# Kernel tuning notes

Hardware: AMD Instinct MI355X
Metric: run time of the kernel (lower is better)

The kernel has to match this reference:

```python
import jax, jax.numpy as jnp
import numpy as np

N, F, H, K = 4096, 512, 256, 8
NEG = -1e9


def _attention(h, mask, a_w, a_b):
    # h: [N,H]; mask: [N,N] bool; a_w: [K,2H]; a_b: [K]
    # per-head logits[i,j] = lrelu(a_src . h_i + a_dst . h_j + b), softmax over
    # neighbors j (A[i,j]==1); out_i = h_i + sum_j alpha_ij h_j; isolated nodes
    # (no neighbors) keep h_i unchanged (alpha row masked to zero).
    Hd = h.shape[1]
    src = h @ a_w[:, :Hd].T + a_b[None, :]   # [N,K]
    dst = h @ a_w[:, Hd:].T                  # [N,K]
    fmask = mask.astype(h.dtype)
    outs = []
    for k in range(a_w.shape[0]):
        logits = jax.nn.leaky_relu(src[:, k][:, None] + dst[:, k][None, :], 0.01)
        logits = jnp.where(mask, logits, NEG)
        alpha = jax.nn.softmax(logits, axis=1) * fmask  # zero rows for isolated nodes
        outs.append(h + alpha @ h)
    return outs


def setup_inputs() -> dict:
    key = jax.random.key(0)
    ks = jax.random.split(key, 12)
    s = 0.02
    adjacency = jax.random.randint(ks[0], (N, N), 0, 2).astype(jnp.float32)
    feats = jax.random.normal(ks[1], (N, F), dtype=jnp.float32)
    return {
        "adjacency": adjacency,
        "feats": feats,
        "W1_w": jax.random.normal(ks[2], (H, F), dtype=jnp.float32) * s,
        "W1_b": jnp.zeros((H,), jnp.float32),
        "a1_w": jax.random.normal(ks[3], (K, 2 * H), dtype=jnp.float32) * s,
        "a1_b": jnp.zeros((K,), jnp.float32),
        "W2_w": jax.random.normal(ks[4], (H, K * H), dtype=jnp.float32) * s,
        "W2_b": jnp.zeros((H,), jnp.float32),
        "a2_w": jax.random.normal(ks[5], (K, 2 * H), dtype=jnp.float32) * s,
        "a2_b": jnp.zeros((K,), jnp.float32),
        "out_w": jax.random.normal(ks[6], (1, H), dtype=jnp.float32) * s,
        "out_b": jnp.zeros((1,), jnp.float32),
    }


def reference(adjacency, feats, W1_w, W1_b, a1_w, a1_b, W2_w, W2_b, a2_w, a2_b, out_w, out_b):
    mask = adjacency == 1.0
    # torch.inner(A, feats.T) == A @ feats; dropout is identity in eval mode
    h1 = (adjacency @ feats) @ W1_w.T + W1_b            # [N,H]
    heads1 = _attention(h1, mask, a1_w, a1_b)           # K x [N,H]
    h1_new = jax.nn.elu(jnp.concatenate(heads1, axis=1))  # [N,K*H]
    h2 = h1_new @ W2_w.T + W2_b                         # [N,H]
    heads2 = _attention(h2, mask, a2_w, a2_b)
    avg = sum(heads2) / a2_w.shape[0]                   # [N,H]
    h2_new = jax.nn.elu(avg)
    avgd = jnp.mean(h2_new, axis=0)                     # [H]
    return avgd @ out_w.T + out_b                       # [1]
```

## Files before the change

kernel.cpp:

```cpp
#include <hip/hip_runtime.h>
#include <hip/hip_bf16.h>
#include <hip/hip_fp16.h>


#define NN 4096
#define FF 512
#define HH 256
#define KK 8
#define KH 2048

typedef __attribute__((ext_vector_type(8))) short bf16x8;
typedef __attribute__((ext_vector_type(4))) float f32x4;
typedef __attribute__((ext_vector_type(16))) float f32x16;
typedef _Float16 h16x2 __attribute__((ext_vector_type(2)));
typedef _Float16 h16x8 __attribute__((ext_vector_type(8)));

__device__ inline short f2bf(float x) {
    __hip_bfloat16 b = __float2bfloat16(x);
    return *reinterpret_cast<short*>(&b);
}
__device__ inline short to_bf(float x) { return f2bf(x); }
__device__ inline short to_bf(short x) { return x; }

__device__ inline unsigned int pkh(float a, float b) {
    auto r = __builtin_amdgcn_cvt_pkrtz(a, b);
    unsigned int u;
    __builtin_memcpy(&u, &r, 4);
    return u;
}
__device__ inline unsigned int h2mul(unsigned int a, unsigned int b) {
    h16x2 av, bv;
    __builtin_memcpy(&av, &a, 4);
    __builtin_memcpy(&bv, &b, 4);
    h16x2 r = av * bv;
    unsigned int u;
    __builtin_memcpy(&u, &r, 4);
    return u;
}
__device__ inline unsigned int h2max(unsigned int a, unsigned int b) {
    h16x2 av, bv;
    __builtin_memcpy(&av, &a, 4);
    __builtin_memcpy(&bv, &b, 4);
    h16x2 r = __builtin_elementwise_max(av, bv);
    unsigned int u;
    __builtin_memcpy(&u, &r, 4);
    return u;
}
__device__ inline float h2dot1(unsigned int a, float c) {
    h16x2 av;
    __builtin_memcpy(&av, &a, 4);
    h16x2 one = {(_Float16)1.0f, (_Float16)1.0f};
    return __builtin_amdgcn_fdot2(av, one, c, false);
}

__device__ inline unsigned int enc_f(float x) {
    unsigned int u = __float_as_uint(x);
    return (u & 0x80000000u) ? ~u : (u | 0x80000000u);
}
__device__ inline float dec_f(unsigned int e) {
    unsigned int u = (e & 0x80000000u) ? (e ^ 0x80000000u) : ~e;
    return __uint_as_float(u);
}

__global__ void pack_mask_kernel(const float* __restrict__ adj,
                                 unsigned int* __restrict__ mbits) {
    int i = blockIdx.x;
    int lane = threadIdx.x & 63;
    int wv = threadIdx.x >> 6;
    for (int j0 = wv * 64; j0 < NN; j0 += 256) {
        float v = adj[(size_t)i * NN + j0 + lane];
        unsigned long long b = __ballot(v == 1.0f);
        if (lane == 0) {
            mbits[i * 128 + (j0 >> 5)]     = (unsigned int)(b & 0xffffffffull);
            mbits[i * 128 + (j0 >> 5) + 1] = (unsigned int)(b >> 32);
        }
    }
}

template <typename T>
__global__ __launch_bounds__(256) void cvt_a_frag_kernel(const T* __restrict__ src,
                                                         bf16x8* __restrict__ dst, int K) {
    int t = threadIdx.x, lane = t & 63, w = t >> 6, mt = blockIdx.x;
    int Kt = K >> 5;
    int m = mt * 16 + (lane & 15), kq = (lane >> 4) * 8;
    for (int kt = w; kt < Kt; kt += 4) {
        size_t base = (size_t)m * K + kt * 32 + kq;
        bf16x8 v;
#pragma unroll
        for (int jj = 0; jj < 8; jj++) v[jj] = to_bf(src[base + jj]);
        dst[((size_t)mt * Kt + kt) * 64 + lane] = v;
    }
}

__global__ __launch_bounds__(256) void cvt_bt_frag_kernel(const float* __restrict__ Wm,
                                                          bf16x8* __restrict__ dst,
                                                          int K, int Nt) {
    int t = threadIdx.x, lane = t & 63, w = t >> 6, nt = blockIdx.x;
    int Kt = K >> 5;
    int n = nt * 16 + (lane & 15), kq = (lane >> 4) * 8;
    for (int kt = w; kt < Kt; kt += 4) {
        size_t base = (size_t)n * K + kt * 32 + kq;
        bf16x8 v;
#pragma unroll
        for (int jj = 0; jj < 8; jj++) v[jj] = f2bf(Wm[base + jj]);
        dst[((size_t)kt * Nt + nt) * 64 + lane] = v;
    }
}

template <int W>
__global__ __launch_bounds__(256) void cvt_b_frag_kernel(const float* __restrict__ src,
                                                         bf16x8* __restrict__ dst) {
    __shared__ float hs[32][W + 8];
    constexpr int Nt = W / 16;
    int t = threadIdx.x, jb = blockIdx.x;
    {
        int r = t >> 3, cb = (t & 7) * (W / 8);
        const float* sp = &src[(size_t)(jb * 32 + r) * W + cb];
#pragma unroll
        for (int q = 0; q < W / 32; q++) *(float4*)&hs[r][cb + q * 4] = *(const float4*)&sp[q * 4];
    }
    __syncthreads();
    for (int id = t; id < Nt * 64; id += 256) {
        int nt = id >> 6, lane = id & 63;
        int c = nt * 16 + (lane & 15), q8 = (lane >> 4) * 8;
        bf16x8 v;
#pragma unroll
        for (int jj = 0; jj < 8; jj++) v[jj] = f2bf(hs[q8 + jj][c]);
        dst[((size_t)jb * Nt + nt) * 64 + lane] = v;
    }
}

__global__ __launch_bounds__(256) void gemm_frag_kernel(
    const bf16x8* __restrict__ Af, const bf16x8* __restrict__ Bf,
    const float* __restrict__ bias, float* __restrict__ C,
    int Kt, int Nt, int Nrow) {
    int t = threadIdx.x, lane = t & 63, w = t >> 6;
    int quad = lane >> 4, c16 = lane & 15;
    int wm = w & 1, wn = w >> 1;
    int mt0 = blockIdx.y * 4 + wm * 2;
    int nt0 = blockIdx.x * 8 + wn * 4;
    f32x4 acc[2][4];
#pragma unroll
    for (int i = 0; i < 2; i++)
#pragma unroll
        for (int j = 0; j < 4; j++) acc[i][j] = (f32x4){0.f, 0.f, 0.f, 0.f};
    const bf16x8* ap = Af + (size_t)mt0 * Kt * 64 + lane;
    const bf16x8* bp = Bf + (size_t)nt0 * 64 + lane;
#pragma unroll 2
    for (int kt = 0; kt < Kt; kt++) {
        bf16x8 a0 = ap[(size_t)kt * 64];
        bf16x8 a1 = ap[((size_t)Kt + kt) * 64];
        bf16x8 b0 = bp[(size_t)kt * Nt * 64];
        bf16x8 b1 = bp[((size_t)kt * Nt + 1) * 64];
        bf16x8 b2 = bp[((size_t)kt * Nt + 2) * 64];
        bf16x8 b3 = bp[((size_t)kt * Nt + 3) * 64];
        acc[0][0] = __builtin_amdgcn_mfma_f32_16x16x32_bf16(a0, b0, acc[0][0], 0, 0, 0);
        acc[0][1] = __builtin_amdgcn_mfma_f32_16x16x32_bf16(a0, b1, acc[0][1], 0, 0, 0);
        acc[0][2] = __builtin_amdgcn_mfma_f32_16x16x32_bf16(a0, b2, acc[0][2], 0, 0, 0);
        acc[0][3] = __builtin_amdgcn_mfma_f32_16x16x32_bf16(a0, b3, acc[0][3], 0, 0, 0);
        acc[1][0] = __builtin_amdgcn_mfma_f32_16x16x32_bf16(a1, b0, acc[1][0], 0, 0, 0);
        acc[1][1] = __builtin_amdgcn_mfma_f32_16x16x32_bf16(a1, b1, acc[1][1], 0, 0, 0);
        acc[1][2] = __builtin_amdgcn_mfma_f32_16x16x32_bf16(a1, b2, acc[1][2], 0, 0, 0);
        acc[1][3] = __builtin_amdgcn_mfma_f32_16x16x32_bf16(a1, b3, acc[1][3], 0, 0, 0);
    }
#pragma unroll
    for (int i = 0; i < 2; i++) {
#pragma unroll
        for (int j = 0; j < 4; j++) {
            int n = (nt0 + j) * 16 + c16;
            float bv = bias ? bias[n] : 0.f;
#pragma unroll
            for (int reg = 0; reg < 4; reg++) {
                int m = (mt0 + i) * 16 + quad * 4 + reg;
                C[(size_t)m * Nrow + n] = acc[i][j][reg] + bv;
            }
        }
    }
}

__global__ __launch_bounds__(256) void gemm_adj_kernel(
    const unsigned int* __restrict__ mbits, const bf16x8* __restrict__ Bf,
    float* __restrict__ C, int Kt, int Nt, int Nrow) {
    int t = threadIdx.x, lane = t & 63, w = t >> 6;
    int quad = lane >> 4, c16 = lane & 15;
    int wm = w & 1, wn = w >> 1;
    int mt0 = blockIdx.y * 4 + wm * 2;
    int nt0 = blockIdx.x * 8 + wn * 4;
    int m = lane & 15, q8 = (lane >> 4) * 8;
    int row0 = mt0 * 16 + m, row1 = row0 + 16;
    f32x4 acc[2][4];
#pragma unroll
    for (int i = 0; i < 2; i++)
#pragma unroll
        for (int j = 0; j < 4; j++) acc[i][j] = (f32x4){0.f, 0.f, 0.f, 0.f};
    const bf16x8* bp = Bf + (size_t)nt0 * 64 + lane;
#pragma unroll 2
    for (int kt = 0; kt < Kt; kt++) {
        unsigned int w0 = mbits[(size_t)row0 * 128 + kt];
        unsigned int w1 = mbits[(size_t)row1 * 128 + kt];
        unsigned int mb0 = (w0 >> q8) & 0xffu;
        unsigned int mb1 = (w1 >> q8) & 0xffu;
        union { unsigned int u[4]; bf16x8 v; } A0, A1;
#pragma unroll
        for (int jp = 0; jp < 4; jp++) {
            unsigned int u0 = (mb0 >> (2 * jp)) & 3u;
            unsigned int u1 = (mb1 >> (2 * jp)) & 3u;
            A0.u[jp] = ((u0 * 0x8001u) & 0x10001u) * 0x3F80u;
            A1.u[jp] = ((u1 * 0x8001u) & 0x10001u) * 0x3F80u;
        }
        bf16x8 b0 = bp[(size_t)kt * Nt * 64];
        bf16x8 b1 = bp[((size_t)kt * Nt + 1) * 64];
        bf16x8 b2 = bp[((size_t)kt * Nt + 2) * 64];
        bf16x8 b3 = bp[((size_t)kt * Nt + 3) * 64];
        acc[0][0] = __builtin_amdgcn_mfma_f32_16x16x32_bf16(A0.v, b0, acc[0][0], 0, 0, 0);
        acc[0][1] = __builtin_amdgcn_mfma_f32_16x16x32_bf16(A0.v, b1, acc[0][1], 0, 0, 0);
        acc[0][2] = __builtin_amdgcn_mfma_f32_16x16x32_bf16(A0.v, b2, acc[0][2], 0, 0, 0);
        acc[0][3] = __builtin_amdgcn_mfma_f32_16x16x32_bf16(A0.v, b3, acc[0][3], 0, 0, 0);
        acc[1][0] = __builtin_amdgcn_mfma_f32_16x16x32_bf16(A1.v, b0, acc[1][0], 0, 0, 0);
        acc[1][1] = __builtin_amdgcn_mfma_f32_16x16x32_bf16(A1.v, b1, acc[1][1], 0, 0, 0);
        acc[1][2] = __builtin_amdgcn_mfma_f32_16x16x32_bf16(A1.v, b2, acc[1][2], 0, 0, 0);
        acc[1][3] = __builtin_amdgcn_mfma_f32_16x16x32_bf16(A1.v, b3, acc[1][3], 0, 0, 0);
    }
#pragma unroll
    for (int i = 0; i < 2; i++) {
#pragma unroll
        for (int j = 0; j < 4; j++) {
            int n = (nt0 + j) * 16 + c16;
#pragma unroll
            for (int reg = 0; reg < 4; reg++) {
                int mm = (mt0 + i) * 16 + quad * 4 + reg;
                C[(size_t)mm * Nrow + n] = acc[i][j][reg];
            }
        }
    }
}

__global__ __launch_bounds__(256) void prep_kernel(const float* __restrict__ h,
                                                   const float* __restrict__ aw,
                                                   const float* __restrict__ ab,
                                                   h16x8* __restrict__ HB16,
                                                   float* __restrict__ srcT,
                                                   float* __restrict__ dstT,
                                                   unsigned int* __restrict__ maxd_u) {
    __shared__ __align__(16) float hs[32][264];
    __shared__ __align__(16) float awl[KK * 512];
    int t = threadIdx.x, jb = blockIdx.x;
#pragma unroll
    for (int q = 0; q < 4; q++)
        *(float4*)&awl[(t + q * 256) * 4] = *(const float4*)&aw[(t + q * 256) * 4];
    {
        int r = t >> 3, cb = (t & 7) * 32;
        const float* hp = &h[(size_t)(jb * 32 + r) * HH + cb];
#pragma unroll
        for (int q = 0; q < 8; q++) *(float4*)&hs[r][cb + q * 4] = *(const float4*)&hp[q * 4];
    }
    __syncthreads();
#pragma unroll
    for (int it = 0; it < 4; it++) {
        int id = t + it * 256;
        int q = id >> 9, nt = (id >> 6) & 7, lane = id & 63;
        int c = nt * 32 + (lane & 31), j8 = q * 16 + (lane >> 5) * 8;
        union { unsigned int u[4]; h16x8 v; } pk;
#pragma unroll
        for (int jp = 0; jp < 4; jp++)
            pk.u[jp] = pkh(hs[j8 + 2 * jp][c], hs[j8 + 2 * jp + 1][c]);
        HB16[((size_t)(jb * 2 + q)) * 512 + nt * 64 + lane] = pk.v;
    }
    {
        const float LOG2E = 1.4426950408889634f;
        int row = t & 31, head = t >> 5;
        float s = ab[head], d = 0.f;
        const float* ws = &awl[head * 512];
        const float* wd = ws + 256;
#pragma unroll 4
        for (int c = 0; c < 256; c += 4) {
            float4 hv = *(const float4*)&hs[row][c];
            float4 a4 = *(const float4*)&ws[c];
            float4 b4 = *(const float4*)&wd[c];
            s += hv.x * a4.x + hv.y * a4.y + hv.z * a4.z + hv.w * a4.w;
            d += hv.x * b4.x + hv.y * b4.y + hv.z * b4.z + hv.w * b4.w;
        }
        float ds = d * LOG2E;
        srcT[head * NN + jb * 32 + row] = s * LOG2E;
        dstT[head * NN + jb * 32 + row] = ds;
        float mx = ds;
#pragma unroll
        for (int off = 16; off > 0; off >>= 1) mx = fmaxf(mx, __shfl_xor(mx, off));
        if (row == 0) atomicMax(&maxd_u[head], enc_f(mx));
    }
}

template <int MODE>
__global__ __launch_bounds__(256, 2) void attn32_kernel(
    const float* __restrict__ h, const float* __restrict__ srcT,
    const float* __restrict__ dstT, const unsigned int* __restrict__ maxd_u,
    const unsigned int* __restrict__ mbits, const h16x8* __restrict__ HB16,
    void* __restrict__ outp) {
    __shared__ __align__(16) char smraw[49600];
    __shared__ float l_all[2][2][32];
    __shared__ float linv_l[2][32];
    unsigned short* e1t = (unsigned short*)smraw;
    unsigned short* e2t = (unsigned short*)(smraw + 16384);
    unsigned int* mrow = (unsigned int*)(smraw + 32768);
    float* accbuf = (float*)smraw;

    int t = threadIdx.x;
    int i0 = blockIdx.x * 32;
    int k0 = blockIdx.y * 2;

    float Dv0 = dec_f(maxd_u[k0]), Dv1 = dec_f(maxd_u[k0 + 1]);
#pragma unroll
    for (int q = 0; q < 8; q++) {
        int idx = t + q * 256;
        int hh = idx >> 10, off = (idx & 1023) * 4;
        float D = hh ? Dv1 : Dv0;
        float4 dv = *(const float4*)&dstT[(size_t)(k0 + hh) * NN + off];
        float d0 = dv.x - D, d1 = dv.y - D, d2 = dv.z - D, d3 = dv.w - D;
        uint2 p1, p2;
        p1.x = pkh(__builtin_amdgcn_exp2f(d0), __builtin_amdgcn_exp2f(d1));
        p1.y = pkh(__builtin_amdgcn_exp2f(d2), __builtin_amdgcn_exp2f(d3));
        p2.x = pkh(__builtin_amdgcn_exp2f(0.01f * d0), __builtin_amdgcn_exp2f(0.01f * d1));
        p2.y = pkh(__builtin_amdgcn_exp2f(0.01f * d2), __builtin_amdgcn_exp2f(0.01f * d3));
        *(uint2*)&e1t[hh * 4096 + off] = p1;
        *(uint2*)&e2t[hh * 4096 + off] = p2;
    }
#pragma unroll
    for (int q = 0; q < 16; q++) {
        int idx = t + q * 256;
        int r = idx >> 7, wd = idx & 127;
        mrow[r * 131 + wd] = mbits[(size_t)(i0 + r) * 128 + wd];
    }
    __syncthreads();

    int lane = t & 63, w = t >> 6;
    int jh = w & 1, ch = w >> 1;
    int rowl = lane & 31, jsub = (lane >> 5) * 8;

    unsigned int AcPk[2], BcPk[2];
    float lacc[2] = {0.f, 0.f};
#pragma unroll
    for (int hh = 0; hh < 2; hh++) {
        float sL = srcT[(size_t)(k0 + hh) * NN + i0 + rowl];
        float xm = sL + (hh ? Dv1 : Dv0);
        float mL = fmaxf(xm, 0.01f * xm);
        float Acf = __builtin_amdgcn_exp2f(xm - mL);
        float Bcf = __builtin_amdgcn_exp2f(fmaf(0.01f, xm, -mL));
        AcPk[hh] = pkh(Acf, Acf);
        BcPk[hh] = pkh(Bcf, Bcf);
    }

    f32x16 acc[2][4];
#pragma unroll
    for (int hh = 0; hh < 2; hh++)
#pragma unroll
        for (int nt = 0; nt < 4; nt++)
#pragma unroll
            for (int r = 0; r < 16; r++) acc[hh][nt][r] = 0.f;

    const unsigned short* e1b0 = e1t;
    const unsigned short* e1b1 = e1t + 4096;
    const unsigned short* e2b0 = e2t;
    const unsigned short* e2b1 = e2t + 4096;

    for (int jj0 = 0; jj0 < 64; jj0++) {
        int jbg = jh * 64 + jj0;
        unsigned int word = mrow[rowl * 131 + jbg];
#pragma unroll
        for (int s = 0; s < 2; s++) {
            int j16 = jbg * 2 + s;
            unsigned int mb = (word >> (s * 16 + jsub)) & 0xffu;
            unsigned int mw[4];
#pragma unroll
            for (int jp = 0; jp < 4; jp++) {
                unsigned int u2 = (mb >> (2 * jp)) & 3u;
                mw[jp] = ((u2 * 0x8001u) & 0x10001u) * 0xffffu;
            }
            int eoff = j16 * 16 + jsub;
            union { unsigned int u[4]; h16x8 v; } P[2];
            {
                uint4 E1 = *(const uint4*)&e1b0[eoff];
                uint4 E2 = *(const uint4*)&e2b0[eoff];
                unsigned int v0 = h2max(h2mul(E1.x, AcPk[0]), h2mul(E2.x, BcPk[0])) & mw[0];
                unsigned int v1 = h2max(h2mul(E1.y, AcPk[0]), h2mul(E2.y, BcPk[0])) & mw[1];
                unsigned int v2 = h2max(h2mul(E1.z, AcPk[0]), h2mul(E2.z, BcPk[0])) & mw[2];
                unsigned int v3 = h2max(h2mul(E1.w, AcPk[0]), h2mul(E2.w, BcPk[0])) & mw[3];
                lacc[0] = h2dot1(v0, lacc[0]);
                lacc[0] = h2dot1(v1, lacc[0]);
                lacc[0] = h2dot1(v2, lacc[0]);
                lacc[0] = h2dot1(v3, lacc[0]);
                P[0].u[0] = v0; P[0].u[1] = v1; P[0].u[2] = v2; P[0].u[3] = v3;
            }
            {
                uint4 E1 = *(const uint4*)&e1b1[eoff];
                uint4 E2 = *(const uint4*)&e2b1[eoff];
                unsigned int v0 = h2max(h2mul(E1.x, AcPk[1]), h2mul(E2.x, BcPk[1])) & mw[0];
                unsigned int v1 = h2max(h2mul(E1.y, AcPk[1]), h2mul(E2.y, BcPk[1])) & mw[1];
                unsigned int v2 = h2max(h2mul(E1.z, AcPk[1]), h2mul(E2.z, BcPk[1])) & mw[2];
                unsigned int v3 = h2max(h2mul(E1.w, AcPk[1]), h2mul(E2.w, BcPk[1])) & mw[3];
                lacc[1] = h2dot1(v0, lacc[1]);
                lacc[1] = h2dot1(v1, lacc[1]);
                lacc[1] = h2dot1(v2, lacc[1]);
                lacc[1] = h2dot1(v3, lacc[1]);
                P[1].u[0] = v0; P[1].u[1] = v1; P[1].u[2] = v2; P[1].u[3] = v3;
            }
            const h16x8* bp = &HB16[(size_t)j16 * 512 + (ch * 4) * 64 + lane];
#pragma unroll
            for (int nt = 0; nt < 4; nt++) {
                h16x8 bv = bp[nt * 64];
                acc[0][nt] = __builtin_amdgcn_mfma_f32_32x32x16_f16(P[0].v, bv, acc[0][nt], 0, 0, 0);
                acc[1][nt] = __builtin_amdgcn_mfma_f32_32x32x16_f16(P[1].v, bv, acc[1][nt], 0, 0, 0);
            }
        }
    }

    lacc[0] += __shfl_xor(lacc[0], 32);
    lacc[1] += __shfl_xor(lacc[1], 32);
    if (ch == 0 && lane < 32) {
        l_all[jh][0][lane] = lacc[0];
        l_all[jh][1][lane] = lacc[1];
    }
    __syncthreads();
    if (t < 32) {
#pragma unroll
        for (int hh = 0; hh < 2; hh++) {
            float lt = l_all[0][hh][t] + l_all[1][hh][t];
            linv_l[hh][t] = (lt > 0.f) ? 1.f / lt : 0.f;
        }
    }
    __syncthreads();

#pragma unroll
    for (int r = 0; r < 2; r++) {
        if (jh == 1) {
#pragma unroll
            for (int nt = 0; nt < 4; nt++) {
                float* dp = accbuf + (size_t)((ch * 4 + nt) * 16) * 64 + lane;
#pragma unroll
                for (int reg = 0; reg < 16; reg++) dp[reg * 64] = acc[r][nt][reg];
            }
        }
        __syncthreads();
        if (jh == 0) {
            int khead = k0 + r;
#pragma unroll
            for (int nt = 0; nt < 4; nt++) {
                const float* sp = accbuf + (size_t)((ch * 4 + nt) * 16) * 64 + lane;
                int c = (ch * 4 + nt) * 32 + (lane & 31);
#pragma unroll
                for (int reg = 0; reg < 16; reg++) {
                    int rowloc = (reg & 3) + 8 * (reg >> 2) + 4 * (lane >> 5);
                    float v = (acc[r][nt][reg] + sp[reg * 64]) * linv_l[r][rowloc];
                    int i = i0 + rowloc;
                    if (MODE == 1) {
                        v += h[(size_t)i * HH + c];
                        v = (v > 0.f) ? v : (__expf(v) - 1.f);
                        ((short*)outp)[(size_t)i * KH + (size_t)khead * HH + c] = f2bf(v);
                    } else {
                        ((short*)outp)[(size_t)khead * NN * HH + (size_t)i * HH + c] = f2bf(v);
                    }
                }
            }
        }
        if (r == 0) __syncthreads();
    }
}

__global__ void colsum_kernel(const float* __restrict__ h2,
                              const short* __restrict__ heads,
                              float* __restrict__ partial) {
    int c = threadIdx.x;
    int b = blockIdx.x;
    float s = 0.f;
    for (int il = 0; il < 64; il++) {
        int i = b * 64 + il;
        float v = h2[(size_t)i * HH + c];
#pragma unroll
        for (int k = 0; k < KK; k++) {
            unsigned int bits = (unsigned int)(unsigned short)heads[(size_t)k * NN * HH + (size_t)i * HH + c];
            v += 0.125f * __uint_as_float(bits << 16);
        }
        s += (v > 0.f) ? v : (__expf(v) - 1.f);
    }
    partial[b * HH + c] = s;
}

__global__ void final_kernel(const float* __restrict__ partial,
                             const float* __restrict__ out_w,
                             const float* __restrict__ out_b,
                             float* __restrict__ dout) {
    __shared__ float red[256];
    int c = threadIdx.x;
    float s = 0.f;
    for (int b = 0; b < 64; b++) s += partial[b * HH + c];
    red[c] = (s / 4096.f) * out_w[c];
    __syncthreads();
    for (int off = 128; off > 0; off >>= 1) {
        if (c < off) red[c] += red[c + off];
        __syncthreads();
    }
    if (c == 0) dout[0] = red[0] + out_b[0];
}

extern "C" void kernel_launch(void* const* d_in, const int* in_sizes, int n_in,
                              void* d_out, int out_size, void* d_ws, size_t ws_size,
                              hipStream_t stream) {
    (void)in_sizes; (void)n_in; (void)out_size; (void)ws_size;
    const float* adj   = (const float*)d_in[0];
    const float* feats = (const float*)d_in[1];
    const float* W1_w  = (const float*)d_in[2];
    const float* W1_b  = (const float*)d_in[3];
    const float* a1_w  = (const float*)d_in[4];
    const float* a1_b  = (const float*)d_in[5];
    const float* W2_w  = (const float*)d_in[6];
    const float* W2_b  = (const float*)d_in[7];
    const float* a2_w  = (const float*)d_in[8];
    const float* a2_b  = (const float*)d_in[9];
    const float* out_w = (const float*)d_in[10];
    const float* out_b = (const float*)d_in[11];

    char* w = (char*)d_ws;
    const size_t MB = 1ull << 20;
    unsigned int* mbits = (unsigned int*)(w);
    short*  h1nb   = (short*)(w + 2 * MB);
    bf16x8* h1na   = (bf16x8*)(w + 18 * MB);
    short*  planes = (short*)(w + 2 * MB);
    bf16x8* Bfeats = (bf16x8*)(w + 34 * MB);
    float*  h2     = (float*)(w + 34 * MB);
    float*  tmp1   = (float*)(w + 38 * MB);
    float*  h1     = (float*)(w + 38 * MB);
    bf16x8* W1f    = (bf16x8*)(w + 42 * MB);
    bf16x8* W2f    = (bf16x8*)(w + 42 * MB + 256 * 1024);
    float*  srcT   = (float*)(w + 43 * MB + 256 * 1024);
    float*  dstT   = (float*)(w + 43 * MB + 384 * 1024);
    unsigned int* maxd_u = (unsigned int*)(w + 43 * MB + 512 * 1024);
    h16x8*  HB16   = (h16x8*)(w + 44 * MB);
    bf16x8* tmp1a  = (bf16x8*)(w + 46 * MB);
    float*  partial = (float*)(w + 50 * MB);

    pack_mask_kernel<<<NN, 256, 0, stream>>>(adj, mbits);
    cvt_b_frag_kernel<FF><<<NN / 32, 256, 0, stream>>>(feats, Bfeats);
    gemm_adj_kernel<<<dim3(FF / 128, NN / 64), 256, 0, stream>>>(
        mbits, Bfeats, tmp1, NN / 32, FF / 16, FF);
    cvt_a_frag_kernel<float><<<NN / 16, 256, 0, stream>>>(tmp1, tmp1a, FF);
    cvt_bt_frag_kernel<<<HH / 16, 256, 0, stream>>>(W1_w, W1f, FF, HH / 16);
    gemm_frag_kernel<<<dim3(HH / 128, NN / 64), 256, 0, stream>>>(
        tmp1a, W1f, W1_b, h1, FF / 32, HH / 16, HH);

    (void)hipMemsetAsync(maxd_u, 0, KK * sizeof(unsigned int), stream);
    prep_kernel<<<NN / 32, 256, 0, stream>>>(h1, a1_w, a1_b, HB16, srcT, dstT, maxd_u);
    attn32_kernel<1><<<dim3(NN / 32, KK / 2), 256, 0, stream>>>(
        h1, srcT, dstT, maxd_u, mbits, HB16, h1nb);
    cvt_a_frag_kernel<short><<<NN / 16, 256, 0, stream>>>(h1nb, h1na, KH);
    cvt_bt_frag_kernel<<<HH / 16, 256, 0, stream>>>(W2_w, W2f, KH, HH / 16);
    gemm_frag_kernel<<<dim3(HH / 128, NN / 64), 256, 0, stream>>>(
        h1na, W2f, W2_b, h2, KH / 32, HH / 16, HH);

    (void)hipMemsetAsync(maxd_u, 0, KK * sizeof(unsigned int), stream);
    prep_kernel<<<NN / 32, 256, 0, stream>>>(h2, a2_w, a2_b, HB16, srcT, dstT, maxd_u);
    attn32_kernel<2><<<dim3(NN / 32, KK / 2), 256, 0, stream>>>(
        h2, srcT, dstT, maxd_u, mbits, HB16, planes);
    colsum_kernel<<<64, 256, 0, stream>>>(h2, planes, partial);
    final_kernel<<<1, 256, 0, stream>>>(partial, out_w, out_b, (float*)d_out);
}
```

Baseline: 462.8 us.

## Process one attention head per block instead of two; widen colsum grid

The attention kernel now handles a single head per block and launches twice as many blocks (grid y = K instead of K/2). Each block needs half the LDS for the exp tables and half the accumulator registers, which should allow more occupancy and more parallel blocks. The cost is that the mask row load and the HB16 B-fragment loads are no longer shared across two heads, so global/LDS traffic per MFMA roughly doubles. The colsum reduction also uses 256 blocks of 16 rows instead of 64 blocks of 64 rows, with the final kernel summing 256 partials.

```diff
diff --git a/kernel.cpp b/kernel.cpp
--- a/kernel.cpp
+++ b/kernel.cpp
@@ -296,33 +296,32 @@
     const float* __restrict__ dstT, const unsigned int* __restrict__ maxd_u,
     const unsigned int* __restrict__ mbits, const h16x8* __restrict__ HB16,
     void* __restrict__ outp) {
-    __shared__ __align__(16) char smraw[49600];
-    __shared__ float l_all[2][2][32];
-    __shared__ float linv_l[2][32];
+    __shared__ __align__(16) char smraw[33536];
+    __shared__ float l_all[2][32];
+    __shared__ float linv_l[32];
     unsigned short* e1t = (unsigned short*)smraw;
-    unsigned short* e2t = (unsigned short*)(smraw + 16384);
-    unsigned int* mrow = (unsigned int*)(smraw + 32768);
+    unsigned short* e2t = (unsigned short*)(smraw + 8192);
+    unsigned int* mrow = (unsigned int*)(smraw + 16384);
     float* accbuf = (float*)smraw;
 
     int t = threadIdx.x;
     int i0 = blockIdx.x * 32;
-    int k0 = blockIdx.y * 2;
-
-    float Dv0 = dec_f(maxd_u[k0]), Dv1 = dec_f(maxd_u[k0 + 1]);
-#pragma unroll
-    for (int q = 0; q < 8; q++) {
+    int khead = blockIdx.y;
+
+    float Dv = dec_f(maxd_u[khead]);
+#pragma unroll
+    for (int q = 0; q < 4; q++) {
         int idx = t + q * 256;
-        int hh = idx >> 10, off = (idx & 1023) * 4;
-        float D = hh ? Dv1 : Dv0;
-        float4 dv = *(const float4*)&dstT[(size_t)(k0 + hh) * NN + off];
-        float d0 = dv.x - D, d1 = dv.y - D, d2 = dv.z - D, d3 = dv.w - D;
+        int off = idx * 4;
+        float4 dv = *(const float4*)&dstT[(size_t)khead * NN + off];
+        float d0 = dv.x - Dv, d1 = dv.y - Dv, d2 = dv.z - Dv, d3 = dv.w - Dv;
         uint2 p1, p2;
         p1.x = pkh(__builtin_amdgcn_exp2f(d0), __builtin_amdgcn_exp2f(d1));
         p1.y = pkh(__builtin_amdgcn_exp2f(d2), __builtin_amdgcn_exp2f(d3));
         p2.x = pkh(__builtin_amdgcn_exp2f(0.01f * d0), __builtin_amdgcn_exp2f(0.01f * d1));
         p2.y = pkh(__builtin_amdgcn_exp2f(0.01f * d2), __builtin_amdgcn_exp2f(0.01f * d3));
-        *(uint2*)&e1t[hh * 4096 + off] = p1;
-        *(uint2*)&e2t[hh * 4096 + off] = p2;
+        *(uint2*)&e1t[off] = p1;
+        *(uint2*)&e2t[off] = p2;
     }
 #pragma unroll
     for (int q = 0; q < 16; q++) {
@@ -336,31 +335,23 @@
     int jh = w & 1, ch = w >> 1;
     int rowl = lane & 31, jsub = (lane >> 5) * 8;
 
-    unsigned int AcPk[2], BcPk[2];
-    float lacc[2] = {0.f, 0.f};
-#pragma unroll
-    for (int hh = 0; hh < 2; hh++) {
-        float sL = srcT[(size_t)(k0 + hh) * NN + i0 + rowl];
-        float xm = sL + (hh ? Dv1 : Dv0);
+    unsigned int AcPk, BcPk;
+    float lacc = 0.f;
+    {
+        float sL = srcT[(size_t)khead * NN + i0 + rowl];
+        float xm = sL + Dv;
         float mL = fmaxf(xm, 0.01f * xm);
         float Acf = __builtin_amdgcn_exp2f(xm - mL);
         float Bcf = __builtin_amdgcn_exp2f(fmaf(0.01f, xm, -mL));
-        AcPk[hh] = pkh(Acf, Acf);
-        BcPk[hh] = pkh(Bcf, Bcf);
-    }
-
-    f32x16 acc[2][4];
-#pragma unroll
-    for (int hh = 0; hh < 2; hh++)
-#pragma unroll
-        for (int nt = 0; nt < 4; nt++)
-#pragma unroll
-            for (int r = 0; r < 16; r++) acc[hh][nt][r] = 0.f;
-
-    const unsigned short* e1b0 = e1t;
-    const unsigned short* e1b1 = e1t + 4096;
-    const unsigned short* e2b0 = e2t;
-    const unsigned short* e2b1 = e2t + 4096;
+        AcPk = pkh(Acf, Acf);
+        BcPk = pkh(Bcf, Bcf);
+    }
+
+    f32x16 acc[4];
+#pragma unroll
+    for (int nt = 0; nt < 4; nt++)
+#pragma unroll
+        for (int r = 0; r < 16; r++) acc[nt][r] = 0.f;
 
     for (int jj0 = 0; jj0 < 64; jj0++) {
         int jbg = jh * 64 + jj0;
@@ -376,92 +367,64 @@
                 mw[jp] = ((u2 * 0x8001u) & 0x10001u) * 0xffffu;
             }
             int eoff = j16 * 16 + jsub;
-            union { unsigned int u[4]; h16x8 v; } P[2];
+            union { unsigned int u[4]; h16x8 v; } P;
             {
-                uint4 E1 = *(const uint4*)&e1b0[eoff];
-                uint4 E2 = *(const uint4*)&e2b0[eoff];
-                unsigned int v0 = h2max(h2mul(E1.x, AcPk[0]), h2mul(E2.x, BcPk[0])) & mw[0];
-                unsigned int v1 = h2max(h2mul(E1.y, AcPk[0]), h2mul(E2.y, BcPk[0])) & mw[1];
-                unsigned int v2 = h2max(h2mul(E1.z, AcPk[0]), h2mul(E2.z, BcPk[0])) & mw[2];
-                unsigned int v3 = h2max(h2mul(E1.w, AcPk[0]), h2mul(E2.w, BcPk[0])) & mw[3];
-                lacc[0] = h2dot1(v0, lacc[0]);
-                lacc[0] = h2dot1(v1, lacc[0]);
-                lacc[0] = h2dot1(v2, lacc[0]);
-                lacc[0] = h2dot1(v3, lacc[0]);
-                P[0].u[0] = v0; P[0].u[1] = v1; P[0].u[2] = v2; P[0].u[3] = v3;
-            }
-            {
-                uint4 E1 = *(const uint4*)&e1b1[eoff];
-                uint4 E2 = *(const uint4*)&e2b1[eoff];
-                unsigned int v0 = h2max(h2mul(E1.x, AcPk[1]), h2mul(E2.x, BcPk[1])) & mw[0];
-                unsigned int v1 = h2max(h2mul(E1.y, AcPk[1]), h2mul(E2.y, BcPk[1])) & mw[1];
-                unsigned int v2 = h2max(h2mul(E1.z, AcPk[1]), h2mul(E2.z, BcPk[1])) & mw[2];
-                unsigned int v3 = h2max(h2mul(E1.w, AcPk[1]), h2mul(E2.w, BcPk[1])) & mw[3];
-                lacc[1] = h2dot1(v0, lacc[1]);
-                lacc[1] = h2dot1(v1, lacc[1]);
-                lacc[1] = h2dot1(v2, lacc[1]);
-                lacc[1] = h2dot1(v3, lacc[1]);
-                P[1].u[0] = v0; P[1].u[1] = v1; P[1].u[2] = v2; P[1].u[3] = v3;
+                uint4 E1 = *(const uint4*)&e1t[eoff];
+                uint4 E2 = *(const uint4*)&e2t[eoff];
+                unsigned int v0 = h2max(h2mul(E1.x, AcPk), h2mul(E2.x, BcPk)) & mw[0];
+                unsigned int v1 = h2max(h2mul(E1.y, AcPk), h2mul(E2.y, BcPk)) & mw[1];
+                unsigned int v2 = h2max(h2mul(E1.z, AcPk), h2mul(E2.z, BcPk)) & mw[2];
+                unsigned int v3 = h2max(h2mul(E1.w, AcPk), h2mul(E2.w, BcPk)) & mw[3];
+                lacc = h2dot1(v0, lacc);
+                lacc = h2dot1(v1, lacc);
+                lacc = h2dot1(v2, lacc);
+                lacc = h2dot1(v3, lacc);
+                P.u[0] = v0; P.u[1] = v1; P.u[2] = v2; P.u[3] = v3;
             }
             const h16x8* bp = &HB16[(size_t)j16 * 512 + (ch * 4) * 64 + lane];
 #pragma unroll
             for (int nt = 0; nt < 4; nt++) {
                 h16x8 bv = bp[nt * 64];
-                acc[0][nt] = __builtin_amdgcn_mfma_f32_32x32x16_f16(P[0].v, bv, acc[0][nt], 0, 0, 0);
-                acc[1][nt] = __builtin_amdgcn_mfma_f32_32x32x16_f16(P[1].v, bv, acc[1][nt], 0, 0, 0);
+                acc[nt] = __builtin_amdgcn_mfma_f32_32x32x16_f16(P.v, bv, acc[nt], 0, 0, 0);
             }
         }
     }
 
-    lacc[0] += __shfl_xor(lacc[0], 32);
-    lacc[1] += __shfl_xor(lacc[1], 32);
-    if (ch == 0 && lane < 32) {
-        l_all[jh][0][lane] = lacc[0];
-        l_all[jh][1][lane] = lacc[1];
-    }
+    lacc += __shfl_xor(lacc, 32);
+    if (ch == 0 && lane < 32) l_all[jh][lane] = lacc;
     __syncthreads();
     if (t < 32) {
-#pragma unroll
-        for (int hh = 0; hh < 2; hh++) {
-            float lt = l_all[0][hh][t] + l_all[1][hh][t];
-            linv_l[hh][t] = (lt > 0.f) ? 1.f / lt : 0.f;
+        float lt = l_all[0][t] + l_all[1][t];
+        linv_l[t] = (lt > 0.f) ? 1.f / lt : 0.f;
+    }
+    if (jh == 1) {
+#pragma unroll
+        for (int nt = 0; nt < 4; nt++) {
+            float* dp = accbuf + (size_t)((ch * 4 + nt) * 16) * 64 + lane;
+#pragma unroll
+            for (int reg = 0; reg < 16; reg++) dp[reg * 64] = acc[nt][reg];
         }
     }
     __syncthreads();
-
-#pragma unroll
-    for (int r = 0; r < 2; r++) {
-        if (jh == 1) {
-#pragma unroll
-            for (int nt = 0; nt < 4; nt++) {
-                float* dp = accbuf + (size_t)((ch * 4 + nt) * 16) * 64 + lane;
-#pragma unroll
-                for (int reg = 0; reg < 16; reg++) dp[reg * 64] = acc[r][nt][reg];
-            }
-        }
-        __syncthreads();
-        if (jh == 0) {
-            int khead = k0 + r;
-#pragma unroll
-            for (int nt = 0; nt < 4; nt++) {
-                const float* sp = accbuf + (size_t)((ch * 4 + nt) * 16) * 64 + lane;
-                int c = (ch * 4 + nt) * 32 + (lane & 31);
-#pragma unroll
-                for (int reg = 0; reg < 16; reg++) {
-                    int rowloc = (reg & 3) + 8 * (reg >> 2) + 4 * (lane >> 5);
-                    float v = (acc[r][nt][reg] + sp[reg * 64]) * linv_l[r][rowloc];
-                    int i = i0 + rowloc;
-                    if (MODE == 1) {
-                        v += h[(size_t)i * HH + c];
-                        v = (v > 0.f) ? v : (__expf(v) - 1.f);
-                        ((short*)outp)[(size_t)i * KH + (size_t)khead * HH + c] = f2bf(v);
-                    } else {
-                        ((short*)outp)[(size_t)khead * NN * HH + (size_t)i * HH + c] = f2bf(v);
-                    }
+    if (jh == 0) {
+#pragma unroll
+        for (int nt = 0; nt < 4; nt++) {
+            const float* sp = accbuf + (size_t)((ch * 4 + nt) * 16) * 64 + lane;
+            int c = (ch * 4 + nt) * 32 + (lane & 31);
+#pragma unroll
+            for (int reg = 0; reg < 16; reg++) {
+                int rowloc = (reg & 3) + 8 * (reg >> 2) + 4 * (lane >> 5);
+                float v = (acc[nt][reg] + sp[reg * 64]) * linv_l[rowloc];
+                int i = i0 + rowloc;
+                if (MODE == 1) {
+                    v += h[(size_t)i * HH + c];
+                    v = (v > 0.f) ? v : (__expf(v) - 1.f);
+                    ((short*)outp)[(size_t)i * KH + (size_t)khead * HH + c] = f2bf(v);
+                } else {
+                    ((short*)outp)[(size_t)khead * NN * HH + (size_t)i * HH + c] = f2bf(v);
                 }
             }
         }
-        if (r == 0) __syncthreads();
     }
 }
 
@@ -471,8 +434,8 @@
     int c = threadIdx.x;
     int b = blockIdx.x;
     float s = 0.f;
-    for (int il = 0; il < 64; il++) {
-        int i = b * 64 + il;
+    for (int il = 0; il < 16; il++) {
+        int i = b * 16 + il;
         float v = h2[(size_t)i * HH + c];
 #pragma unroll
         for (int k = 0; k < KK; k++) {
@@ -491,7 +454,7 @@
     __shared__ float red[256];
     int c = threadIdx.x;
     float s = 0.f;
-    for (int b = 0; b < 64; b++) s += partial[b * HH + c];
+    for (int b = 0; b < 256; b++) s += partial[b * HH + c];
     red[c] = (s / 4096.f) * out_w[c];
     __syncthreads();
     for (int off = 128; off > 0; off >>= 1) {
@@ -548,7 +511,7 @@
 
     (void)hipMemsetAsync(maxd_u, 0, KK * sizeof(unsigned int), stream);
     prep_kernel<<<NN / 32, 256, 0, stream>>>(h1, a1_w, a1_b, HB16, srcT, dstT, maxd_u);
-    attn32_kernel<1><<<dim3(NN / 32, KK / 2), 256, 0, stream>>>(
+    attn32_kernel<1><<<dim3(NN / 32, KK), 256, 0, stream>>>(
         h1, srcT, dstT, maxd_u, mbits, HB16, h1nb);
     cvt_a_frag_kernel<short><<<NN / 16, 256, 0, stream>>>(h1nb, h1na, KH);
     cvt_bt_frag_kernel<<<HH / 16, 256, 0, stream>>>(W2_w, W2f, KH, HH / 16);
@@ -557,8 +520,8 @@
 
     (void)hipMemsetAsync(maxd_u, 0, KK * sizeof(unsigned int), stream);
     prep_kernel<<<NN / 32, 256, 0, stream>>>(h2, a2_w, a2_b, HB16, srcT, dstT, maxd_u);
-    attn32_kernel<2><<<dim3(NN / 32, KK / 2), 256, 0, stream>>>(
+    attn32_kernel<2><<<dim3(NN / 32, KK), 256, 0, stream>>>(
         h2, srcT, dstT, maxd_u, mbits, HB16, planes);
-    colsum_kernel<<<64, 256, 0, stream>>>(h2, planes, partial);
+    colsum_kernel<<<256, 256, 0, stream>>>(h2, planes, partial);
     final_kernel<<<1, 256, 0, stream>>>(partial, out_w, out_b, (float*)d_out);
 }
```

New measurement: 608.2 us. 31.4% more time.
